# Performance work log

Hardware: AMD Instinct MI355X
Metric: run time of the kernel (lower is better)

The kernel has to match this reference:

```python
import jax, jax.numpy as jnp
import numpy as np

B = 16384          # number of positions (segments)
TOT = 491520       # total active features per color (~30 per position)
NF = 768           # 2*6*64 feature space


def setup_inputs() -> dict:
    key = jax.random.key(0)
    ks = jax.random.split(key, 10)
    white_features = jax.random.randint(ks[0], (TOT,), 0, NF)
    white_indices = jnp.sort(jax.random.randint(ks[1], (TOT,), 0, B)).at[-1].set(B - 1)
    black_features = jax.random.randint(ks[2], (TOT,), 0, NF)
    black_indices = jnp.sort(jax.random.randint(ks[3], (TOT,), 0, B)).at[-1].set(B - 1)
    W1 = jax.random.normal(ks[4], (64, NF), dtype=jnp.float32) * 0.05
    b1 = jax.random.normal(ks[5], (64,), dtype=jnp.float32) * 0.05
    W2 = jax.random.normal(ks[6], (32, 128), dtype=jnp.float32) * 0.05
    b2 = jax.random.normal(ks[7], (32,), dtype=jnp.float32) * 0.05
    W3 = jax.random.normal(ks[8], (1, 32), dtype=jnp.float32) * 0.05
    b3 = jax.random.normal(ks[9], (1,), dtype=jnp.float32) * 0.05
    return {
        "white_features": white_features, "white_indices": white_indices,
        "black_features": black_features, "black_indices": black_indices,
        "W1": W1, "b1": b1, "W2": W2, "b2": b2, "W3": W3, "b3": b3,
        "num_segments": B,
    }


def reference(white_features, white_indices, black_features, black_indices,
              W1, b1, W2, b2, W3, b3, num_segments):
    W1T = W1.T  # [NF, 64]

    def feed_l1(feats, idx):
        f = jnp.take(W1T, feats, axis=0)                       # [TOT, 64] gather
        a = jax.ops.segment_sum(f, idx, num_segments=num_segments)  # [B, 64]
        return a + b1

    a1w = feed_l1(white_features, white_indices)
    a1b = feed_l1(black_features, black_indices)
    a1 = jnp.clip(jnp.concatenate([a1w, a1b], axis=1), 0.0, 1.0)  # hardtanh(0,1)
    a2 = jnp.clip(a1 @ W2.T + b2, 0.0, 1.0)
    a3 = jax.nn.sigmoid(a2 @ W3.T + b3)
    return a3.squeeze(-1)
```

## Files before the change

kernel.cpp:

```cpp
#include <hip/hip_runtime.h>
#include <hip/hip_fp16.h>
#include <math.h>

#define NPOS 16384
#define NTOT 491520
#define NFEAT 768
#define DUMMY 768
#define PITCH 68

typedef _Float16 h2 __attribute__((ext_vector_type(2)));

__device__ __forceinline__ int imin(int a, int b) { return a < b ? a : b; }
__device__ __forceinline__ float clamp01(float x) { return fminf(fmaxf(x, 0.f), 1.f); }

#if __has_builtin(__builtin_amdgcn_fdot2)
#define FDOT2(a, b, c) __builtin_amdgcn_fdot2((a), (b), (c), false)
#else
#define FDOT2(a, b, c) ((c) + (float)(a)[0] * (float)(b)[0] + (float)(a)[1] * (float)(b)[1])
#endif

__device__ __forceinline__ h2 toh2(__half2 x) { return __builtin_bit_cast(h2, x); }

__global__ __launch_bounds__(1024, 4) void k_all(
    const int* __restrict__ wf, const int* __restrict__ bf,
    const int* __restrict__ wi, const int* __restrict__ bi,
    const float* __restrict__ W1, const float4* __restrict__ b1q,
    const float* __restrict__ W2, const float* __restrict__ b2,
    const float* __restrict__ W3, const float* __restrict__ b3,
    float* __restrict__ out)
{
    __shared__ __half  w1t[769 * PITCH];
    __shared__ __half2 w2t[2048];
    __shared__ __align__(16) int ivs[16][64];
    __shared__ uint4   a1sq[16][16];
    __shared__ int     sb[2][65];

    int t = threadIdx.x;
    int wave = t >> 6, lane = t & 63;
    int p0 = blockIdx.x * 64;

    if (wave < 14) {
        int r = lane;
        const float* wrow = W1 + r * NFEAT;
#pragma unroll 2
        for (int i = 0; i < 14; ++i) {
            int f4 = wave + 14 * i;
            if (f4 >= 192) break;
            float4 v = *(const float4*)&wrow[f4 * 4];
            int fb = f4 * 4;
            w1t[(fb + 0) * PITCH + r] = __float2half(v.x);
            w1t[(fb + 1) * PITCH + r] = __float2half(v.y);
            w1t[(fb + 2) * PITCH + r] = __float2half(v.z);
            w1t[(fb + 3) * PITCH + r] = __float2half(v.w);
        }
    } else {
        const int* __restrict__ arr = (wave == 14) ? wi : bi;
        int col = wave - 14;
        int t1 = p0 + lane, t2 = p0 + 64;
        int lo1 = 0, hi1 = 0, g1 = 0;
        int lo2 = 0, hi2 = 0, g2 = 0;
        if (t1 > 0) { hi1 = NTOT; g1 = imin(t1 * 30, NTOT - 1); }
        if (t2 < NPOS) { hi2 = NTOT; g2 = imin(t2 * 30, NTOT - 1); }
        else { lo2 = NTOT; hi2 = NTOT; }
#pragma unroll 1
        for (int it = 0; it < 8; ++it) {
            bool c1 = lo1 < hi1, c2 = lo2 < hi2;
            if (!c1 && !c2) break;
            int v1 = 0, v2 = 0;
            if (c1) v1 = arr[g1];
            if (c2) v2 = arr[g2];
            if (c1) {
                if (v1 < t1) lo1 = g1 + 1; else hi1 = g1;
                int ng = g1 + (t1 - v1) * 30;
                if (ng < lo1 || ng >= hi1) ng = lo1 + ((hi1 - lo1) >> 1);
                g1 = ng;
            }
            if (c2) {
                if (v2 < t2) lo2 = g2 + 1; else hi2 = g2;
                int ng = g2 + (t2 - v2) * 30;
                if (ng < lo2 || ng >= hi2) ng = lo2 + ((hi2 - lo2) >> 1);
                g2 = ng;
            }
        }
#pragma unroll 1
        for (;;) {
            bool c1 = lo1 < hi1, c2 = lo2 < hi2;
            if (!c1 && !c2) break;
            int m1 = 0, m2 = 0, v1 = 0, v2 = 0;
            if (c1) { m1 = lo1 + ((hi1 - lo1) >> 1); v1 = arr[m1]; }
            if (c2) { m2 = lo2 + ((hi2 - lo2) >> 1); v2 = arr[m2]; }
            if (c1) { if (v1 < t1) lo1 = m1 + 1; else hi1 = m1; }
            if (c2) { if (v2 < t2) lo2 = m2 + 1; else hi2 = m2; }
        }
        sb[col][lane] = lo1;
        if (lane == 63) sb[col][64] = lo2;

        int tl = t - 896;
        for (int x = tl; x < 2048; x += 128) {
            int i = x >> 5, jj = x & 31;
            w2t[x] = __floats2half2_rn(W2[jj * 128 + 2 * i], W2[jj * 128 + 2 * i + 1]);
        }
        if (tl < 64) w1t[DUMMY * PITCH + tl] = __float2half(0.f);
    }
    __syncthreads();

    int g = lane >> 4, k = lane & 15;
    int j = lane & 31, h = lane >> 5;

    h2 w2r[32];
#pragma unroll
    for (int i = 0; i < 32; ++i) w2r[i] = toh2(w2t[(h * 32 + i) * 32 + j]);

    float4 bb = b1q[k];
    float b2j = b2[j], w3j = W3[j], b30 = b3[0];

    int* myiv = &ivs[wave][0];
    __half2* a1h = (__half2*)&a1sq[wave][0];

    for (int it = 0; it < 4; ++it) {
        int pl = wave + 16 * it;
        int pos = p0 + pl;
        int ws_ = sb[0][pl], we = sb[0][pl + 1];
        int bs_ = sb[1][pl], be = sb[1][pl + 1];

        float wa0 = 0.f, wa1 = 0.f, wa2 = 0.f, wa3 = 0.f;
        float ba0 = 0.f, ba1 = 0.f, ba2 = 0.f, ba3 = 0.f;

        auto run = [&](const int* __restrict__ feats, int s, int e,
                       float& A0, float& A1, float& A2, float& A3) {
            for (int tt = s; tt < e; tt += 64) {
                myiv[lane] = (tt + lane < e) ? feats[tt + lane] : DUMMY;
                int nc = (imin(e - tt, 64) + 15) >> 4;
                for (int c = 0; c < nc; ++c) {
                    uint4 iq = *(const uint4*)&myiv[c * 16 + g * 4];
                    uint2 d0 = *(const uint2*)&w1t[(int)iq.x * PITCH + k * 4];
                    uint2 d1 = *(const uint2*)&w1t[(int)iq.y * PITCH + k * 4];
                    uint2 d2 = *(const uint2*)&w1t[(int)iq.z * PITCH + k * 4];
                    uint2 d3 = *(const uint2*)&w1t[(int)iq.w * PITCH + k * 4];
                    h2 l0 = __builtin_bit_cast(h2, d0.x), u0 = __builtin_bit_cast(h2, d0.y);
                    h2 l1 = __builtin_bit_cast(h2, d1.x), u1 = __builtin_bit_cast(h2, d1.y);
                    h2 l2 = __builtin_bit_cast(h2, d2.x), u2 = __builtin_bit_cast(h2, d2.y);
                    h2 l3 = __builtin_bit_cast(h2, d3.x), u3 = __builtin_bit_cast(h2, d3.y);
                    A0 += (float)l0[0] + (float)l1[0] + (float)l2[0] + (float)l3[0];
                    A1 += (float)l0[1] + (float)l1[1] + (float)l2[1] + (float)l3[1];
                    A2 += (float)u0[0] + (float)u1[0] + (float)u2[0] + (float)u3[0];
                    A3 += (float)u0[1] + (float)u1[1] + (float)u2[1] + (float)u3[1];
                }
            }
        };
        run(wf, ws_, we, wa0, wa1, wa2, wa3);
        run(bf, bs_, be, ba0, ba1, ba2, ba3);

        wa0 += __shfl_xor(wa0, 16); wa0 += __shfl_xor(wa0, 32);
        wa1 += __shfl_xor(wa1, 16); wa1 += __shfl_xor(wa1, 32);
        wa2 += __shfl_xor(wa2, 16); wa2 += __shfl_xor(wa2, 32);
        wa3 += __shfl_xor(wa3, 16); wa3 += __shfl_xor(wa3, 32);
        ba0 += __shfl_xor(ba0, 16); ba0 += __shfl_xor(ba0, 32);
        ba1 += __shfl_xor(ba1, 16); ba1 += __shfl_xor(ba1, 32);
        ba2 += __shfl_xor(ba2, 16); ba2 += __shfl_xor(ba2, 32);
        ba3 += __shfl_xor(ba3, 16); ba3 += __shfl_xor(ba3, 32);

        if (lane < 32) {
            __half2 q0, q1;
            if (g == 0) {
                q0 = __floats2half2_rn(clamp01(wa0 + bb.x), clamp01(wa1 + bb.y));
                q1 = __floats2half2_rn(clamp01(wa2 + bb.z), clamp01(wa3 + bb.w));
            } else {
                q0 = __floats2half2_rn(clamp01(ba0 + bb.x), clamp01(ba1 + bb.y));
                q1 = __floats2half2_rn(clamp01(ba2 + bb.z), clamp01(ba3 + bb.w));
            }
            a1h[g * 32 + k * 2]     = q0;
            a1h[g * 32 + k * 2 + 1] = q1;
        }

        const uint4* aq = &a1sq[wave][h * 8];
        float acc = 0.f;
#pragma unroll
        for (int q4 = 0; q4 < 8; ++q4) {
            uint4 qq = aq[q4];
            acc = FDOT2(__builtin_bit_cast(h2, qq.x), w2r[q4 * 4 + 0], acc);
            acc = FDOT2(__builtin_bit_cast(h2, qq.y), w2r[q4 * 4 + 1], acc);
            acc = FDOT2(__builtin_bit_cast(h2, qq.z), w2r[q4 * 4 + 2], acc);
            acc = FDOT2(__builtin_bit_cast(h2, qq.w), w2r[q4 * 4 + 3], acc);
        }
        acc += __shfl_xor(acc, 32);

        float a2v = clamp01(acc + b2j);
        float p = a2v * w3j;
        p += __shfl_xor(p, 16);
        p += __shfl_xor(p, 8);
        p += __shfl_xor(p, 4);
        p += __shfl_xor(p, 2);
        p += __shfl_xor(p, 1);
        if (lane == 0)
            out[pos] = 1.f / (1.f + __expf(-(p + b30)));
    }
}

extern "C" void kernel_launch(void* const* d_in, const int* in_sizes, int n_in,
                              void* d_out, int out_size, void* d_ws, size_t ws_size,
                              hipStream_t stream) {
    const int*   wf = (const int*)d_in[0];
    const int*   wi = (const int*)d_in[1];
    const int*   bf = (const int*)d_in[2];
    const int*   bi = (const int*)d_in[3];
    const float* W1 = (const float*)d_in[4];
    const float* b1 = (const float*)d_in[5];
    const float* W2 = (const float*)d_in[6];
    const float* b2 = (const float*)d_in[7];
    const float* W3 = (const float*)d_in[8];
    const float* b3 = (const float*)d_in[9];
    float* out = (float*)d_out;

    k_all<<<NPOS / 64, 1024, 0, stream>>>(wf, bf, wi, bi, W1, (const float4*)b1,
                                          W2, b2, W3, b3, out);
}
```

Measured before the change: 27.42 us.

## Prefetch next position's feature indices and interleave white/black gathers with fdot2 accumulation

Each wave now loads the feature indices for its next position into registers while it processes the current one, which hides global-load latency behind the LDS gather work. The white and black gather chunks are interleaved in a single loop to expose more independent LDS loads. The half-to-float adds are replaced by perm-packed fdot2 with a ones vector, cutting the number of convert and add instructions. The cost is extra registers and LDS for a second index buffer, plus fallback loops for segments longer than 64 features.

```diff
diff --git a/kernel.cpp b/kernel.cpp
--- a/kernel.cpp
+++ b/kernel.cpp
@@ -17,6 +17,14 @@
 #define FDOT2(a, b, c) __builtin_amdgcn_fdot2((a), (b), (c), false)
 #else
 #define FDOT2(a, b, c) ((c) + (float)(a)[0] * (float)(b)[0] + (float)(a)[1] * (float)(b)[1])
+#endif
+
+#if __has_builtin(__builtin_amdgcn_perm)
+#define PACK_LO(x, y) __builtin_amdgcn_perm((y), (x), 0x05040100u)
+#define PACK_HI(x, y) __builtin_amdgcn_perm((y), (x), 0x07060302u)
+#else
+#define PACK_LO(x, y) (((x) & 0xFFFFu) | ((y) << 16))
+#define PACK_HI(x, y) (((x) >> 16) | ((y) & 0xFFFF0000u))
 #endif
 
 __device__ __forceinline__ h2 toh2(__half2 x) { return __builtin_bit_cast(h2, x); }
@@ -31,7 +39,7 @@
 {
     __shared__ __half  w1t[769 * PITCH];
     __shared__ __half2 w2t[2048];
-    __shared__ __align__(16) int ivs[16][64];
+    __shared__ __align__(16) int ivs[16][2][64];
     __shared__ uint4   a1sq[16][16];
     __shared__ int     sb[2][65];
 
@@ -107,6 +115,11 @@
     int g = lane >> 4, k = lane & 15;
     int j = lane & 31, h = lane >> 5;
 
+    int ws_ = sb[0][wave], we = sb[0][wave + 1];
+    int bs_ = sb[1][wave], be = sb[1][wave + 1];
+    int nivw = (ws_ + lane < we) ? wf[ws_ + lane] : DUMMY;
+    int nivb = (bs_ + lane < be) ? bf[bs_ + lane] : DUMMY;
+
     h2 w2r[32];
 #pragma unroll
     for (int i = 0; i < 32; ++i) w2r[i] = toh2(w2t[(h * 32 + i) * 32 + j]);
@@ -114,42 +127,64 @@
     float4 bb = b1q[k];
     float b2j = b2[j], w3j = W3[j], b30 = b3[0];
 
-    int* myiv = &ivs[wave][0];
+    const h2 ones = {(_Float16)1.0f, (_Float16)1.0f};
+    int* ivW = &ivs[wave][0][0];
+    int* ivB = &ivs[wave][1][0];
     __half2* a1h = (__half2*)&a1sq[wave][0];
+
+    auto CHUNK = [&](const int* __restrict__ miv, int c,
+                     float& A0, float& A1, float& A2, float& A3) {
+        uint4 iq = *(const uint4*)&miv[c * 16 + g * 4];
+        uint2 d0 = *(const uint2*)&w1t[(int)iq.x * PITCH + k * 4];
+        uint2 d1 = *(const uint2*)&w1t[(int)iq.y * PITCH + k * 4];
+        uint2 d2 = *(const uint2*)&w1t[(int)iq.z * PITCH + k * 4];
+        uint2 d3 = *(const uint2*)&w1t[(int)iq.w * PITCH + k * 4];
+        A0 = FDOT2(__builtin_bit_cast(h2, PACK_LO(d0.x, d1.x)), ones, A0);
+        A1 = FDOT2(__builtin_bit_cast(h2, PACK_HI(d0.x, d1.x)), ones, A1);
+        A2 = FDOT2(__builtin_bit_cast(h2, PACK_LO(d0.y, d1.y)), ones, A2);
+        A3 = FDOT2(__builtin_bit_cast(h2, PACK_HI(d0.y, d1.y)), ones, A3);
+        A0 = FDOT2(__builtin_bit_cast(h2, PACK_LO(d2.x, d3.x)), ones, A0);
+        A1 = FDOT2(__builtin_bit_cast(h2, PACK_HI(d2.x, d3.x)), ones, A1);
+        A2 = FDOT2(__builtin_bit_cast(h2, PACK_LO(d2.y, d3.y)), ones, A2);
+        A3 = FDOT2(__builtin_bit_cast(h2, PACK_HI(d2.y, d3.y)), ones, A3);
+    };
 
     for (int it = 0; it < 4; ++it) {
         int pl = wave + 16 * it;
         int pos = p0 + pl;
-        int ws_ = sb[0][pl], we = sb[0][pl + 1];
-        int bs_ = sb[1][pl], be = sb[1][pl + 1];
+
+        ivW[lane] = nivw;
+        ivB[lane] = nivb;
+        int cws = ws_, cwe = we, cbs = bs_, cbe = be;
+
+        if (it < 3) {
+            int npl = pl + 16;
+            ws_ = sb[0][npl]; we = sb[0][npl + 1];
+            bs_ = sb[1][npl]; be = sb[1][npl + 1];
+            nivw = (ws_ + lane < we) ? wf[ws_ + lane] : DUMMY;
+            nivb = (bs_ + lane < be) ? bf[bs_ + lane] : DUMMY;
+        }
 
         float wa0 = 0.f, wa1 = 0.f, wa2 = 0.f, wa3 = 0.f;
         float ba0 = 0.f, ba1 = 0.f, ba2 = 0.f, ba3 = 0.f;
 
-        auto run = [&](const int* __restrict__ feats, int s, int e,
-                       float& A0, float& A1, float& A2, float& A3) {
-            for (int tt = s; tt < e; tt += 64) {
-                myiv[lane] = (tt + lane < e) ? feats[tt + lane] : DUMMY;
-                int nc = (imin(e - tt, 64) + 15) >> 4;
-                for (int c = 0; c < nc; ++c) {
-                    uint4 iq = *(const uint4*)&myiv[c * 16 + g * 4];
-                    uint2 d0 = *(const uint2*)&w1t[(int)iq.x * PITCH + k * 4];
-                    uint2 d1 = *(const uint2*)&w1t[(int)iq.y * PITCH + k * 4];
-                    uint2 d2 = *(const uint2*)&w1t[(int)iq.z * PITCH + k * 4];
-                    uint2 d3 = *(const uint2*)&w1t[(int)iq.w * PITCH + k * 4];
-                    h2 l0 = __builtin_bit_cast(h2, d0.x), u0 = __builtin_bit_cast(h2, d0.y);
-                    h2 l1 = __builtin_bit_cast(h2, d1.x), u1 = __builtin_bit_cast(h2, d1.y);
-                    h2 l2 = __builtin_bit_cast(h2, d2.x), u2 = __builtin_bit_cast(h2, d2.y);
-                    h2 l3 = __builtin_bit_cast(h2, d3.x), u3 = __builtin_bit_cast(h2, d3.y);
-                    A0 += (float)l0[0] + (float)l1[0] + (float)l2[0] + (float)l3[0];
-                    A1 += (float)l0[1] + (float)l1[1] + (float)l2[1] + (float)l3[1];
-                    A2 += (float)u0[0] + (float)u1[0] + (float)u2[0] + (float)u3[0];
-                    A3 += (float)u0[1] + (float)u1[1] + (float)u2[1] + (float)u3[1];
-                }
-            }
-        };
-        run(wf, ws_, we, wa0, wa1, wa2, wa3);
-        run(bf, bs_, be, ba0, ba1, ba2, ba3);
+        int ncw = (imin(cwe - cws, 64) + 15) >> 4;
+        int ncb = (imin(cbe - cbs, 64) + 15) >> 4;
+        int ncm = ncw > ncb ? ncw : ncb;
+        for (int c = 0; c < ncm; ++c) {
+            if (c < ncw) CHUNK(ivW, c, wa0, wa1, wa2, wa3);
+            if (c < ncb) CHUNK(ivB, c, ba0, ba1, ba2, ba3);
+        }
+        for (int tt = cws + 64; tt < cwe; tt += 64) {
+            ivW[lane] = (tt + lane < cwe) ? wf[tt + lane] : DUMMY;
+            int nc = (imin(cwe - tt, 64) + 15) >> 4;
+            for (int c = 0; c < nc; ++c) CHUNK(ivW, c, wa0, wa1, wa2, wa3);
+        }
+        for (int tt = cbs + 64; tt < cbe; tt += 64) {
+            ivB[lane] = (tt + lane < cbe) ? bf[tt + lane] : DUMMY;
+            int nc = (imin(cbe - tt, 64) + 15) >> 4;
+            for (int c = 0; c < nc; ++c) CHUNK(ivB, c, ba0, ba1, ba2, ba3);
+        }
 
         wa0 += __shfl_xor(wa0, 16); wa0 += __shfl_xor(wa0, 32);
         wa1 += __shfl_xor(wa1, 16); wa1 += __shfl_xor(wa1, 32);
```

Result: faster. 26.45 us (-3.5%).
